# Optimization experiments

Hardware: AMD Instinct MI355X
Metric: run time of the kernel (lower is better)

Reference implementation:

```python
import jax, jax.numpy as jnp
import numpy as np

B, C, INTER, H, W = 8, 256, 128, 64, 64

def setup_inputs() -> dict:
    key = jax.random.key(0)
    ks = jax.random.split(key, 9)
    s = 0.02
    return {
        "x": jax.random.normal(ks[0], (B, C, H, W), dtype=jnp.float32),
        "Wg": jax.random.normal(ks[1], (INTER, C), dtype=jnp.float32) * s,
        "bg": jax.random.normal(ks[2], (INTER,), dtype=jnp.float32) * s,
        "Wt": jax.random.normal(ks[3], (INTER, C), dtype=jnp.float32) * s,
        "bt": jax.random.normal(ks[4], (INTER,), dtype=jnp.float32) * s,
        "Wp": jax.random.normal(ks[5], (INTER, C), dtype=jnp.float32) * s,
        "bp": jax.random.normal(ks[6], (INTER,), dtype=jnp.float32) * s,
        "Wm": jax.random.normal(ks[7], (C, INTER), dtype=jnp.float32) * s,
        "bm": jax.random.normal(ks[8], (C,), dtype=jnp.float32) * s,
    }

def reference(x, Wg, bg, Wt, bt, Wp, bp, Wm, bm):
    # x: [B, C, H, W]; 1x1 convs are channel GEMMs.
    b, c, h, w = x.shape
    n = h * w
    def conv1x1(inp, Wc, bc):
        return jnp.einsum('bchw,oc->bohw', inp, Wc) + bc[None, :, None, None]
    g_x = conv1x1(x, Wg, bg).reshape(b, -1, n).transpose(0, 2, 1)      # [B, N, d]
    theta_x = conv1x1(x, Wt, bt).reshape(b, -1, n).transpose(0, 2, 1)  # [B, N, d]
    phi_x = conv1x1(x, Wp, bp).reshape(b, -1, n)                       # [B, d, N]
    scores = jnp.einsum('bnd,bdm->bnm', theta_x, phi_x)               # [B, N, N]
    attn = jax.nn.softmax(scores, axis=-1)
    y = jnp.einsum('bnm,bmd->bnd', attn, g_x)                          # [B, N, d]
    y = y.transpose(0, 2, 1).reshape(b, -1, h, w)                      # [B, d, H, W]
    mask = conv1x1(y, Wm, bm)                                          # [B, C, H, W]
    return mask + x
```

## Files before the change

### kernel.cpp

```cpp
#include <hip/hip_runtime.h>
#include <hip/hip_bf16.h>
#include <math.h>

#define BATCH 8
#define CH    256
#define DIM   128
#define NSP   4096

using bf16 = __hip_bfloat16;
typedef __attribute__((ext_vector_type(8))) short bf16x8;
typedef __attribute__((ext_vector_type(4))) float f32x4;

__device__ __forceinline__ unsigned short f2b(float f) {
  return __builtin_bit_cast(unsigned short, __float2bfloat16(f));
}

__device__ __forceinline__ float fexp2(float x) {
  float r;
  asm("v_exp_f32 %0, %1" : "=v"(r) : "v"(x));
  return r;
}

__device__ __forceinline__ void gload16(const void* g, void* l) {
  __builtin_amdgcn_global_load_lds(
      (const __attribute__((address_space(1))) unsigned int*)g,
      (__attribute__((address_space(3))) unsigned int*)l, 16, 0, 0);
}

__global__ __launch_bounds__(256) void k_weights(const float* __restrict__ Wg,
                                                 const float* __restrict__ Wt,
                                                 const float* __restrict__ Wp,
                                                 const float* __restrict__ Wm,
                                                 bf16* __restrict__ Wcat,
                                                 bf16* __restrict__ Wmb) {
  int i = blockIdx.x * 256 + threadIdx.x;
  if (i < 3 * DIM * CH) {
    const float* src = (i < 32768) ? Wg : (i < 65536 ? Wt : Wp);
    Wcat[i] = __float2bfloat16(src[i & 32767]);
  }
  if (i < CH * DIM) Wmb[i] = __float2bfloat16(Wm[i]);
}

__global__ __launch_bounds__(256) void k_transpose(const float* __restrict__ x,
                                                   bf16* __restrict__ xbT) {
  __shared__ __align__(16) float tile[64][68];
  const int b = blockIdx.z, ct = blockIdx.y, nt = blockIdx.x;
  const int t = threadIdx.x;
  const int tr = t >> 4;
  const int tc = t & 15;
  const float* src = x + ((size_t)b * CH + ct * 64) * NSP + nt * 64;
  #pragma unroll
  for (int p = 0; p < 4; ++p) {
    int c = p * 16 + tr;
    float4 v = *(const float4*)(src + (size_t)c * NSP + tc * 4);
    *(float4*)(&tile[c][tc * 4]) = v;
  }
  __syncthreads();
  bf16* dst = xbT + ((size_t)b * NSP + nt * 64) * CH + ct * 64;
  #pragma unroll
  for (int p = 0; p < 4; ++p) {
    int n = p * 16 + tr;
    ushort4 pk;
    pk.x = f2b(tile[tc * 4 + 0][n]);
    pk.y = f2b(tile[tc * 4 + 1][n]);
    pk.z = f2b(tile[tc * 4 + 2][n]);
    pk.w = f2b(tile[tc * 4 + 3][n]);
    *(ushort4*)(dst + (size_t)n * CH + tc * 4) = pk;
  }
}

__global__ __launch_bounds__(256) void k_proj(const bf16* __restrict__ Wcat,
                                              const bf16* __restrict__ xbT,
                                              const float* __restrict__ bg,
                                              const float* __restrict__ bt,
                                              const float* __restrict__ bp,
                                              bf16* __restrict__ theta,
                                              bf16* __restrict__ phi,
                                              bf16* __restrict__ gT) {
  __shared__ __align__(16) char lds[32768];
  const int b = blockIdx.z, p = blockIdx.y, nt = blockIdx.x;
  const int tid = threadIdx.x;
  const int l = tid & 63, w = tid >> 6;
  const int wm = w >> 1, wn = w & 1;
  const int lr = l & 15, lh = l >> 4;
  const int ldsw = (tid & ~63) << 4;

  f32x4 acc[4][4];
  #pragma unroll
  for (int i = 0; i < 4; ++i)
    #pragma unroll
    for (int j = 0; j < 4; ++j) acc[i][j] = (f32x4){0.f, 0.f, 0.f, 0.f};

  const bf16* Asrc = Wcat + (size_t)p * DIM * CH;
  const bf16* Bsrc = xbT + ((size_t)b * NSP + nt * 128) * CH;

  for (int kt = 0; kt < 4; ++kt) {
    const int k0 = kt * 64;
    #pragma unroll
    for (int cc = 0; cc < 4; ++cc) {
      int t = cc * 256 + tid;
      int row = t >> 3, g = t & 7;
      gload16(Asrc + (size_t)row * CH + k0 + ((g ^ (row & 7)) << 3),
              lds + cc * 4096 + ldsw);
      gload16(Bsrc + (size_t)row * CH + k0 + ((g ^ (row & 7)) << 3),
              lds + 16384 + cc * 4096 + ldsw);
    }
    __syncthreads();
    #pragma unroll
    for (int kk = 0; kk < 2; ++kk) {
      bf16x8 af[4], bfr[4];
      #pragma unroll
      for (int mf = 0; mf < 4; ++mf) {
        int row = wm * 64 + mf * 16 + lr;
        int g = kk * 4 + lh;
        af[mf] = *(const bf16x8*)(lds + row * 128 + ((g ^ (row & 7)) << 4));
      }
      #pragma unroll
      for (int nf = 0; nf < 4; ++nf) {
        int row = wn * 64 + nf * 16 + lr;
        int g = kk * 4 + lh;
        bfr[nf] = *(const bf16x8*)(lds + 16384 + row * 128 + ((g ^ (row & 7)) << 4));
      }
      #pragma unroll
      for (int mf = 0; mf < 4; ++mf)
        #pragma unroll
        for (int nf = 0; nf < 4; ++nf)
          acc[mf][nf] = __builtin_amdgcn_mfma_f32_16x16x32_bf16(af[mf], bfr[nf],
                                                                acc[mf][nf], 0, 0, 0);
    }
    __syncthreads();
  }

  const float* bias = (p == 0) ? bg : (p == 1 ? bt : bp);
  bf16* nd = (p == 1) ? theta : phi;
  const float oscale = (p == 1) ? 1.44269504088896f : 1.0f;
  #pragma unroll
  for (int mf = 0; mf < 4; ++mf) {
    const int dbase = wm * 64 + mf * 16 + lh * 4;
    const float4 bv = *(const float4*)(bias + dbase);
    float bvv[4] = {bv.x, bv.y, bv.z, bv.w};
    #pragma unroll
    for (int nf = 0; nf < 4; ++nf) {
      const int n = nt * 128 + wn * 64 + nf * 16 + lr;
      float v[4];
      #pragma unroll
      for (int r = 0; r < 4; ++r) v[r] = (acc[mf][nf][r] + bvv[r]) * oscale;
      if (p == 0) {
        #pragma unroll
        for (int r = 0; r < 4; ++r)
          gT[((size_t)b * DIM + dbase + r) * NSP + n] = __float2bfloat16(v[r]);
      } else {
        ushort4 pk;
        pk.x = f2b(v[0]); pk.y = f2b(v[1]); pk.z = f2b(v[2]); pk.w = f2b(v[3]);
        *(ushort4*)(nd + ((size_t)b * NSP + n) * DIM + dbase) = pk;
      }
    }
  }
}

__global__ __launch_bounds__(512, 2) void k_attn(const bf16* __restrict__ theta,
                                                 const bf16* __restrict__ phi,
                                                 const bf16* __restrict__ gT,
                                                 bf16* __restrict__ y) {
  __shared__ __align__(16) char lds[131072];
  const int b = blockIdx.y, qt = blockIdx.x;
  const int tid = threadIdx.x;
  const int l = tid & 63, w = tid >> 6;
  const int h = w >> 2;
  const int p = w & 3;
  const int lr = l & 15, lh = l >> 4;
  const int tid_h = tid & 255;
  const int ldsw_h = (tid_h & ~63) << 4;

  bf16x8 qf[2][4];
  #pragma unroll
  for (int g = 0; g < 2; ++g) {
    const bf16* qsrc =
        theta + ((size_t)(b * NSP + qt * 128 + p * 32 + g * 16 + lr)) * DIM + lh * 8;
    #pragma unroll
    for (int f = 0; f < 4; ++f) qf[g][f] = *(const bf16x8*)(qsrc + f * 32);
  }

  f32x4 o[2][8];
  #pragma unroll
  for (int g = 0; g < 2; ++g)
    #pragma unroll
    for (int dt = 0; dt < 8; ++dt) o[g][dt] = (f32x4){0.f, 0.f, 0.f, 0.f};
  f32x4 den[2];
  den[0] = (f32x4){0.f, 0.f, 0.f, 0.f};
  den[1] = (f32x4){0.f, 0.f, 0.f, 0.f};

  bf16x8 vones;
  #pragma unroll
  for (int j = 0; j < 8; ++j) vones[j] = (short)0x3F80;

  const bf16* Ksrc = phi + (size_t)b * NSP * DIM;
  const bf16* Vsrc = gT + (size_t)b * DIM * NSP;
  const int kvbase = h * 2048;
  char* const ldsh = lds + h * 65536;

  const bf16* kp[4];
  const bf16* vp[4];
  #pragma unroll
  for (int cc = 0; cc < 4; ++cc) {
    int t = cc * 256 + tid_h;
    int row = t >> 4, g = t & 15;
    int kvs = (row & 32) | (((row >> 2) & 3) << 3) | (((row >> 4) & 1) << 2) |
              (row & 3);
    kp[cc] = Ksrc + (size_t)(kvbase + kvs) * DIM + ((g ^ (row & 7)) << 3);
    int row2 = t >> 3, g2 = t & 7;
    vp[cc] = Vsrc + (size_t)row2 * NSP + kvbase + ((g2 ^ (row2 & 7)) << 3);
  }

  auto stage = [&](int buf) {
    #pragma unroll
    for (int cc = 0; cc < 4; ++cc) {
      gload16(kp[cc], ldsh + buf * 16384 + cc * 4096 + ldsw_h);
      gload16(vp[cc], ldsh + 32768 + buf * 16384 + cc * 4096 + ldsw_h);
      kp[cc] += 64 * DIM;
      vp[cc] += 64;
    }
  };

  stage(0);

  for (int it = 0; it < 32; ++it) {
    if (it < 31) {
      stage((it + 1) & 1);
      asm volatile("s_waitcnt vmcnt(8)" ::: "memory");
    } else {
      asm volatile("s_waitcnt vmcnt(0)" ::: "memory");
    }
    __builtin_amdgcn_s_barrier();
    __builtin_amdgcn_sched_barrier(0);

    const char* Kb = ldsh + (it & 1) * 16384;
    const char* Vb = ldsh + 32768 + (it & 1) * 16384;

    f32x4 sa[2][4];
    #pragma unroll
    for (int g = 0; g < 2; ++g)
      #pragma unroll
      for (int ct = 0; ct < 4; ++ct) sa[g][ct] = (f32x4){0.f, 0.f, 0.f, 0.f};
    #pragma unroll
    for (int ct = 0; ct < 4; ++ct) {
      const int row = ct * 16 + lr;
      #pragma unroll
      for (int f = 0; f < 4; ++f) {
        const int g = f * 4 + lh;
        bf16x8 kf = *(const bf16x8*)(Kb + row * 256 + ((g ^ (row & 7)) << 4));
        sa[0][ct] = __builtin_amdgcn_mfma_f32_16x16x32_bf16(kf, qf[0][f], sa[0][ct], 0, 0, 0);
        sa[1][ct] = __builtin_amdgcn_mfma_f32_16x16x32_bf16(kf, qf[1][f], sa[1][ct], 0, 0, 0);
      }
    }

    #pragma unroll
    for (int ct = 0; ct < 4; ++ct)
      #pragma unroll
      for (int r = 0; r < 4; ++r) {
        sa[0][ct][r] = fexp2(sa[0][ct][r]);
        sa[1][ct][r] = fexp2(sa[1][ct][r]);
      }

    bf16x8 pf[2][2];
    #pragma unroll
    for (int g = 0; g < 2; ++g)
      #pragma unroll
      for (int c = 0; c < 2; ++c) {
        union { bf16x8 v; unsigned short u[8]; } pw;
        #pragma unroll
        for (int u = 0; u < 2; ++u)
          #pragma unroll
          for (int r = 0; r < 4; ++r) pw.u[u * 4 + r] = f2b(sa[g][2 * c + u][r]);
        pf[g][c] = pw.v;
      }

    #pragma unroll
    for (int c = 0; c < 2; ++c) {
      const int gp = c * 4 + lh;
      den[0] = __builtin_amdgcn_mfma_f32_16x16x32_bf16(pf[0][c], vones, den[0], 0, 0, 0);
      den[1] = __builtin_amdgcn_mfma_f32_16x16x32_bf16(pf[1][c], vones, den[1], 0, 0, 0);
      #pragma unroll
      for (int dt = 0; dt < 8; ++dt) {
        const int row = dt * 16 + lr;
        bf16x8 vf = *(const bf16x8*)(Vb + row * 128 + ((gp ^ (row & 7)) << 4));
        o[0][dt] = __builtin_amdgcn_mfma_f32_16x16x32_bf16(pf[0][c], vf, o[0][dt], 0, 0, 0);
        o[1][dt] = __builtin_amdgcn_mfma_f32_16x16x32_bf16(pf[1][c], vf, o[1][dt], 0, 0, 0);
      }
    }

    asm volatile("s_waitcnt lgkmcnt(0)" ::: "memory");
    __builtin_amdgcn_s_barrier();
  }

  {
    #pragma unroll
    for (int g = 0; g < 2; ++g) {
      char* slot = lds + (size_t)((p * 2 + g) * 64 + l) * 144;
      if (h == 1) {
        #pragma unroll
        for (int dt = 0; dt < 8; ++dt) *(f32x4*)(slot + dt * 16) = o[g][dt];
        *(f32x4*)(slot + 128) = den[g];
      }
    }
    __syncthreads();
    if (h == 0) {
      #pragma unroll
      for (int g = 0; g < 2; ++g) {
        char* slot = lds + (size_t)((p * 2 + g) * 64 + l) * 144;
        const f32x4 db = *(const f32x4*)(slot + 128);
        float inv[4];
        #pragma unroll
        for (int r = 0; r < 4; ++r) inv[r] = 1.f / (den[g][r] + db[r]);
        #pragma unroll
        for (int dt = 0; dt < 8; ++dt) {
          const f32x4 ob = *(const f32x4*)(slot + dt * 16);
          const int d = dt * 16 + lr;
          #pragma unroll
          for (int r = 0; r < 4; ++r) {
            const int q = qt * 128 + p * 32 + g * 16 + lh * 4 + r;
            y[(size_t)(b * NSP + q) * DIM + d] =
                __float2bfloat16((o[g][dt][r] + ob[r]) * inv[r]);
          }
        }
      }
    }
  }
}

__global__ __launch_bounds__(256) void k_final(const bf16* __restrict__ Wmb,
                                               const bf16* __restrict__ yb,
                                               const float* __restrict__ bm,
                                               const float* __restrict__ x,
                                               float* __restrict__ out) {
  __shared__ __align__(16) char lds[32768];
  const int b = blockIdx.z, mt = blockIdx.y, nt = blockIdx.x;
  const int tid = threadIdx.x;
  const int l = tid & 63, w = tid >> 6;
  const int wm = w >> 1, wn = w & 1;
  const int lr = l & 15, lh = l >> 4;
  const int ldsw = (tid & ~63) << 4;

  f32x4 acc[4][4];
  #pragma unroll
  for (int i = 0; i < 4; ++i)
    #pragma unroll
    for (int j = 0; j < 4; ++j) acc[i][j] = (f32x4){0.f, 0.f, 0.f, 0.f};

  const bf16* Asrc = Wmb + (size_t)mt * 128 * DIM;
  const bf16* Bsrc = yb + ((size_t)b * NSP + nt * 128) * DIM;

  for (int kt = 0; kt < 2; ++kt) {
    const int k0 = kt * 64;
    #pragma unroll
    for (int cc = 0; cc < 4; ++cc) {
      int t = cc * 256 + tid;
      int row = t >> 3, g = t & 7;
      gload16(Asrc + (size_t)row * DIM + k0 + ((g ^ (row & 7)) << 3),
              lds + cc * 4096 + ldsw);
      gload16(Bsrc + (size_t)row * DIM + k0 + ((g ^ (row & 7)) << 3),
              lds + 16384 + cc * 4096 + ldsw);
    }
    __syncthreads();
    #pragma unroll
    for (int kk = 0; kk < 2; ++kk) {
      bf16x8 af[4], bfr[4];
      #pragma unroll
      for (int mf = 0; mf < 4; ++mf) {
        int row = wm * 64 + mf * 16 + lr;
        int g = kk * 4 + lh;
        af[mf] = *(const bf16x8*)(lds + row * 128 + ((g ^ (row & 7)) << 4));
      }
      #pragma unroll
      for (int nf = 0; nf < 4; ++nf) {
        int row = wn * 64 + nf * 16 + lr;
        int g = kk * 4 + lh;
        bfr[nf] = *(const bf16x8*)(lds + 16384 + row * 128 + ((g ^ (row & 7)) << 4));
      }
      #pragma unroll
      for (int mf = 0; mf < 4; ++mf)
        #pragma unroll
        for (int nf = 0; nf < 4; ++nf)
          acc[mf][nf] = __builtin_amdgcn_mfma_f32_16x16x32_bf16(af[mf], bfr[nf],
                                                                acc[mf][nf], 0, 0, 0);
    }
    __syncthreads();
  }

  #pragma unroll
  for (int mf = 0; mf < 4; ++mf) {
    const int cbase = mt * 128 + wm * 64 + mf * 16 + lh * 4;
    const float4 bv = *(const float4*)(bm + cbase);
    float bvv[4] = {bv.x, bv.y, bv.z, bv.w};
    #pragma unroll
    for (int nf = 0; nf < 4; ++nf) {
      const int n = nt * 128 + wn * 64 + nf * 16 + lr;
      #pragma unroll
      for (int r = 0; r < 4; ++r) {
        const size_t idx = ((size_t)b * CH + cbase + r) * NSP + n;
        out[idx] = acc[mf][nf][r] + bvv[r] + x[idx];
      }
    }
  }
}

extern "C" void kernel_launch(void* const* d_in, const int* in_sizes, int n_in,
                              void* d_out, int out_size, void* d_ws, size_t ws_size,
                              hipStream_t stream) {
  const float* x  = (const float*)d_in[0];
  const float* Wg = (const float*)d_in[1];
  const float* bg = (const float*)d_in[2];
  const float* Wt = (const float*)d_in[3];
  const float* bt = (const float*)d_in[4];
  const float* Wp = (const float*)d_in[5];
  const float* bp = (const float*)d_in[6];
  const float* Wm = (const float*)d_in[7];
  const float* bm = (const float*)d_in[8];
  float* out = (float*)d_out;
  char* ws = (char*)d_ws;

  bf16* xbT   = (bf16*)(ws + 0);
  bf16* Wcat  = (bf16*)(ws + 16777216);
  bf16* Wmb   = (bf16*)(ws + 16973824);
  bf16* theta = (bf16*)(ws + 17039360);
  bf16* phi   = (bf16*)(ws + 25427968);
  bf16* gT    = (bf16*)(ws + 33816576);
  bf16* yb    = (bf16*)(ws + 42205184);

  k_weights  <<<dim3(384),       dim3(256), 0, stream>>>(Wg, Wt, Wp, Wm, Wcat, Wmb);
  k_transpose<<<dim3(64, 4, 8),  dim3(256), 0, stream>>>(x, xbT);
  k_proj     <<<dim3(32, 3, 8),  dim3(256), 0, stream>>>(Wcat, xbT, bg, bt, bp,
                                                         theta, phi, gT);
  k_attn     <<<dim3(32, 8),     dim3(512), 0, stream>>>(theta, phi, gT, yb);
  k_final    <<<dim3(32, 2, 8),  dim3(256), 0, stream>>>(Wmb, yb, bm, x, out);
}
```

Baseline: 199.9 us.

## Fuse weight cast into transpose, reuse x tile across projections, single-stage final GEMM

The weight-conversion kernel is folded into the transpose kernel as an extra z-slice of blocks, which saves one launch. The projection kernel now loads each x tile into LDS once and loops over the three projections, reusing it instead of launching three separate blocks per tile. This cuts the grid from 768 to 256 blocks and raises LDS to 80KB, which may hurt occupancy and parallelism. The final GEMM loads the whole K=128 extent in one stage, dropping one sync round but doubling LDS use.

```diff
diff --git a/kernel.cpp b/kernel.cpp
--- a/kernel.cpp
+++ b/kernel.cpp
@@ -27,22 +27,31 @@
       (__attribute__((address_space(3))) unsigned int*)l, 16, 0, 0);
 }
 
-__global__ __launch_bounds__(256) void k_weights(const float* __restrict__ Wg,
-                                                 const float* __restrict__ Wt,
-                                                 const float* __restrict__ Wp,
-                                                 const float* __restrict__ Wm,
-                                                 bf16* __restrict__ Wcat,
-                                                 bf16* __restrict__ Wmb) {
-  int i = blockIdx.x * 256 + threadIdx.x;
-  if (i < 3 * DIM * CH) {
-    const float* src = (i < 32768) ? Wg : (i < 65536 ? Wt : Wp);
-    Wcat[i] = __float2bfloat16(src[i & 32767]);
-  }
-  if (i < CH * DIM) Wmb[i] = __float2bfloat16(Wm[i]);
-}
-
 __global__ __launch_bounds__(256) void k_transpose(const float* __restrict__ x,
-                                                   bf16* __restrict__ xbT) {
+                                                   bf16* __restrict__ xbT,
+                                                   const float* __restrict__ Wg,
+                                                   const float* __restrict__ Wt,
+                                                   const float* __restrict__ Wp,
+                                                   const float* __restrict__ Wm,
+                                                   bf16* __restrict__ Wcat,
+                                                   bf16* __restrict__ Wmb) {
+  if (blockIdx.z == 8) {
+    int id = (blockIdx.y * 64 + blockIdx.x) * 256 + threadIdx.x;
+    int i2 = id * 2;
+    if (i2 < 3 * DIM * CH) {
+      #pragma unroll
+      for (int e = 0; e < 2; ++e) {
+        int i = i2 + e;
+        const float* src = (i < 32768) ? Wg : (i < 65536 ? Wt : Wp);
+        Wcat[i] = __float2bfloat16(src[i & 32767]);
+      }
+    } else {
+      int k = i2 - 3 * DIM * CH;
+      Wmb[k]     = __float2bfloat16(Wm[k]);
+      Wmb[k + 1] = __float2bfloat16(Wm[k + 1]);
+    }
+    return;
+  }
   __shared__ __align__(16) float tile[64][68];
   const int b = blockIdx.z, ct = blockIdx.y, nt = blockIdx.x;
   const int t = threadIdx.x;
@@ -77,82 +86,91 @@
                                               bf16* __restrict__ theta,
                                               bf16* __restrict__ phi,
                                               bf16* __restrict__ gT) {
-  __shared__ __align__(16) char lds[32768];
-  const int b = blockIdx.z, p = blockIdx.y, nt = blockIdx.x;
+  __shared__ __align__(16) char lds[81920];
+  const int b = blockIdx.y, nt = blockIdx.x;
   const int tid = threadIdx.x;
   const int l = tid & 63, w = tid >> 6;
   const int wm = w >> 1, wn = w & 1;
   const int lr = l & 15, lh = l >> 4;
   const int ldsw = (tid & ~63) << 4;
 
-  f32x4 acc[4][4];
-  #pragma unroll
-  for (int i = 0; i < 4; ++i)
-    #pragma unroll
-    for (int j = 0; j < 4; ++j) acc[i][j] = (f32x4){0.f, 0.f, 0.f, 0.f};
-
-  const bf16* Asrc = Wcat + (size_t)p * DIM * CH;
   const bf16* Bsrc = xbT + ((size_t)b * NSP + nt * 128) * CH;
 
-  for (int kt = 0; kt < 4; ++kt) {
-    const int k0 = kt * 64;
+  #pragma unroll
+  for (int kt = 0; kt < 4; ++kt)
     #pragma unroll
     for (int cc = 0; cc < 4; ++cc) {
       int t = cc * 256 + tid;
       int row = t >> 3, g = t & 7;
-      gload16(Asrc + (size_t)row * CH + k0 + ((g ^ (row & 7)) << 3),
-              lds + cc * 4096 + ldsw);
-      gload16(Bsrc + (size_t)row * CH + k0 + ((g ^ (row & 7)) << 3),
-              lds + 16384 + cc * 4096 + ldsw);
-    }
-    __syncthreads();
-    #pragma unroll
-    for (int kk = 0; kk < 2; ++kk) {
-      bf16x8 af[4], bfr[4];
-      #pragma unroll
-      for (int mf = 0; mf < 4; ++mf) {
-        int row = wm * 64 + mf * 16 + lr;
-        int g = kk * 4 + lh;
-        af[mf] = *(const bf16x8*)(lds + row * 128 + ((g ^ (row & 7)) << 4));
-      }
+      gload16(Bsrc + (size_t)row * CH + kt * 64 + ((g ^ (row & 7)) << 3),
+              lds + kt * 16384 + cc * 4096 + ldsw);
+    }
+
+  for (int p = 0; p < 3; ++p) {
+    f32x4 acc[4][4];
+    #pragma unroll
+    for (int i = 0; i < 4; ++i)
+      #pragma unroll
+      for (int j = 0; j < 4; ++j) acc[i][j] = (f32x4){0.f, 0.f, 0.f, 0.f};
+    const bf16* Asrc = Wcat + (size_t)p * DIM * CH;
+
+    for (int kt = 0; kt < 4; ++kt) {
+      __syncthreads();
+      #pragma unroll
+      for (int cc = 0; cc < 4; ++cc) {
+        int t = cc * 256 + tid;
+        int row = t >> 3, g = t & 7;
+        gload16(Asrc + (size_t)row * CH + kt * 64 + ((g ^ (row & 7)) << 3),
+                lds + 65536 + cc * 4096 + ldsw);
+      }
+      __syncthreads();
+      #pragma unroll
+      for (int kk = 0; kk < 2; ++kk) {
+        bf16x8 af[4], bfr[4];
+        #pragma unroll
+        for (int mf = 0; mf < 4; ++mf) {
+          int row = wm * 64 + mf * 16 + lr;
+          int g = kk * 4 + lh;
+          af[mf] = *(const bf16x8*)(lds + 65536 + row * 128 + ((g ^ (row & 7)) << 4));
+        }
+        #pragma unroll
+        for (int nf = 0; nf < 4; ++nf) {
+          int row = wn * 64 + nf * 16 + lr;
+          int g = kk * 4 + lh;
+          bfr[nf] = *(const bf16x8*)(lds + kt * 16384 + row * 128 + ((g ^ (row & 7)) << 4));
+        }
+        #pragma unroll
+        for (int mf = 0; mf < 4; ++mf)
+          #pragma unroll
+          for (int nf = 0; nf < 4; ++nf)
+            acc[mf][nf] = __builtin_amdgcn_mfma_f32_16x16x32_bf16(af[mf], bfr[nf],
+                                                                  acc[mf][nf], 0, 0, 0);
+      }
+    }
+
+    const float* bias = (p == 0) ? bg : (p == 1 ? bt : bp);
+    bf16* nd = (p == 1) ? theta : phi;
+    const float oscale = (p == 1) ? 1.44269504088896f : 1.0f;
+    #pragma unroll
+    for (int mf = 0; mf < 4; ++mf) {
+      const int dbase = wm * 64 + mf * 16 + lh * 4;
+      const float4 bv = *(const float4*)(bias + dbase);
+      float bvv[4] = {bv.x, bv.y, bv.z, bv.w};
       #pragma unroll
       for (int nf = 0; nf < 4; ++nf) {
-        int row = wn * 64 + nf * 16 + lr;
-        int g = kk * 4 + lh;
-        bfr[nf] = *(const bf16x8*)(lds + 16384 + row * 128 + ((g ^ (row & 7)) << 4));
-      }
-      #pragma unroll
-      for (int mf = 0; mf < 4; ++mf)
-        #pragma unroll
-        for (int nf = 0; nf < 4; ++nf)
-          acc[mf][nf] = __builtin_amdgcn_mfma_f32_16x16x32_bf16(af[mf], bfr[nf],
-                                                                acc[mf][nf], 0, 0, 0);
-    }
-    __syncthreads();
-  }
-
-  const float* bias = (p == 0) ? bg : (p == 1 ? bt : bp);
-  bf16* nd = (p == 1) ? theta : phi;
-  const float oscale = (p == 1) ? 1.44269504088896f : 1.0f;
-  #pragma unroll
-  for (int mf = 0; mf < 4; ++mf) {
-    const int dbase = wm * 64 + mf * 16 + lh * 4;
-    const float4 bv = *(const float4*)(bias + dbase);
-    float bvv[4] = {bv.x, bv.y, bv.z, bv.w};
-    #pragma unroll
-    for (int nf = 0; nf < 4; ++nf) {
-      const int n = nt * 128 + wn * 64 + nf * 16 + lr;
-      float v[4];
-      #pragma unroll
-      for (int r = 0; r < 4; ++r) v[r] = (acc[mf][nf][r] + bvv[r]) * oscale;
-      if (p == 0) {
-        #pragma unroll
-        for (int r = 0; r < 4; ++r)
-          gT[((size_t)b * DIM + dbase + r) * NSP + n] = __float2bfloat16(v[r]);
-      } else {
-        ushort4 pk;
-        pk.x = f2b(v[0]); pk.y = f2b(v[1]); pk.z = f2b(v[2]); pk.w = f2b(v[3]);
-        *(ushort4*)(nd + ((size_t)b * NSP + n) * DIM + dbase) = pk;
+        const int n = nt * 128 + wn * 64 + nf * 16 + lr;
+        float v[4];
+        #pragma unroll
+        for (int r = 0; r < 4; ++r) v[r] = (acc[mf][nf][r] + bvv[r]) * oscale;
+        if (p == 0) {
+          #pragma unroll
+          for (int r = 0; r < 4; ++r)
+            gT[((size_t)b * DIM + dbase + r) * NSP + n] = __float2bfloat16(v[r]);
+        } else {
+          ushort4 pk;
+          pk.x = f2b(v[0]); pk.y = f2b(v[1]); pk.z = f2b(v[2]); pk.w = f2b(v[3]);
+          *(ushort4*)(nd + ((size_t)b * NSP + n) * DIM + dbase) = pk;
+        }
       }
     }
   }
@@ -333,7 +351,7 @@
                                                const float* __restrict__ bm,
                                                const float* __restrict__ x,
                                                float* __restrict__ out) {
-  __shared__ __align__(16) char lds[32768];
+  __shared__ __align__(16) char lds[65536];
   const int b = blockIdx.z, mt = blockIdx.y, nt = blockIdx.x;
   const int tid = threadIdx.x;
   const int l = tid & 63, w = tid >> 6;
@@ -341,50 +359,47 @@
   const int lr = l & 15, lh = l >> 4;
   const int ldsw = (tid & ~63) << 4;
 
-  f32x4 acc[4][4];
-  #pragma unroll
-  for (int i = 0; i < 4; ++i)
-    #pragma unroll
-    for (int j = 0; j < 4; ++j) acc[i][j] = (f32x4){0.f, 0.f, 0.f, 0.f};
-
   const bf16* Asrc = Wmb + (size_t)mt * 128 * DIM;
   const bf16* Bsrc = yb + ((size_t)b * NSP + nt * 128) * DIM;
 
-  for (int kt = 0; kt < 2; ++kt) {
-    const int k0 = kt * 64;
-    #pragma unroll
-    for (int cc = 0; cc < 4; ++cc) {
-      int t = cc * 256 + tid;
-      int row = t >> 3, g = t & 7;
-      gload16(Asrc + (size_t)row * DIM + k0 + ((g ^ (row & 7)) << 3),
-              lds + cc * 4096 + ldsw);
-      gload16(Bsrc + (size_t)row * DIM + k0 + ((g ^ (row & 7)) << 3),
-              lds + 16384 + cc * 4096 + ldsw);
-    }
-    __syncthreads();
-    #pragma unroll
-    for (int kk = 0; kk < 2; ++kk) {
-      bf16x8 af[4], bfr[4];
-      #pragma unroll
-      for (int mf = 0; mf < 4; ++mf) {
-        int row = wm * 64 + mf * 16 + lr;
-        int g = kk * 4 + lh;
-        af[mf] = *(const bf16x8*)(lds + row * 128 + ((g ^ (row & 7)) << 4));
-      }
-      #pragma unroll
-      for (int nf = 0; nf < 4; ++nf) {
-        int row = wn * 64 + nf * 16 + lr;
-        int g = kk * 4 + lh;
-        bfr[nf] = *(const bf16x8*)(lds + 16384 + row * 128 + ((g ^ (row & 7)) << 4));
-      }
-      #pragma unroll
-      for (int mf = 0; mf < 4; ++mf)
-        #pragma unroll
-        for (int nf = 0; nf < 4; ++nf)
-          acc[mf][nf] = __builtin_amdgcn_mfma_f32_16x16x32_bf16(af[mf], bfr[nf],
-                                                                acc[mf][nf], 0, 0, 0);
-    }
-    __syncthreads();
+  #pragma unroll
+  for (int cc = 0; cc < 8; ++cc) {
+    int t = cc * 256 + tid;
+    int row = t >> 4, g = t & 15;
+    gload16(Asrc + (size_t)row * DIM + ((g ^ (row & 7)) << 3),
+            lds + cc * 4096 + ldsw);
+    gload16(Bsrc + (size_t)row * DIM + ((g ^ (row & 7)) << 3),
+            lds + 32768 + cc * 4096 + ldsw);
+  }
+  __syncthreads();
+
+  f32x4 acc[4][4];
+  #pragma unroll
+  for (int i = 0; i < 4; ++i)
+    #pragma unroll
+    for (int j = 0; j < 4; ++j) acc[i][j] = (f32x4){0.f, 0.f, 0.f, 0.f};
+
+  #pragma unroll
+  for (int kk = 0; kk < 4; ++kk) {
+    bf16x8 af[4], bfr[4];
+    #pragma unroll
+    for (int mf = 0; mf < 4; ++mf) {
+      int row = wm * 64 + mf * 16 + lr;
+      int g = kk * 4 + lh;
+      af[mf] = *(const bf16x8*)(lds + row * 256 + ((g ^ (row & 7)) << 4));
+    }
+    #pragma unroll
+    for (int nf = 0; nf < 4; ++nf) {
+      int row = wn * 64 + nf * 16 + lr;
+      int g = kk * 4 + lh;
+      bfr[nf] = *(const bf16x8*)(lds + 32768 + row * 256 + ((g ^ (row & 7)) << 4));
+    }
+    #pragma unroll
+    for (int mf = 0; mf < 4; ++mf)
+      #pragma unroll
+      for (int nf = 0; nf < 4; ++nf)
+        acc[mf][nf] = __builtin_amdgcn_mfma_f32_16x16x32_bf16(af[mf], bfr[nf],
+                                                              acc[mf][nf], 0, 0, 0);
   }
 
   #pragma unroll
@@ -427,9 +442,9 @@
   bf16* gT    = (bf16*)(ws + 33816576);
   bf16* yb    = (bf16*)(ws + 42205184);
 
-  k_weights  <<<dim3(384),       dim3(256), 0, stream>>>(Wg, Wt, Wp, Wm, Wcat, Wmb);
-  k_transpose<<<dim3(64, 4, 8),  dim3(256), 0, stream>>>(x, xbT);
-  k_proj     <<<dim3(32, 3, 8),  dim3(256), 0, stream>>>(Wcat, xbT, bg, bt, bp,
+  k_transpose<<<dim3(64, 4, 9),  dim3(256), 0, stream>>>(x, xbT, Wg, Wt, Wp, Wm,
+                                                         Wcat, Wmb);
+  k_proj     <<<dim3(32, 8),     dim3(256), 0, stream>>>(Wcat, xbT, bg, bt, bp,
                                                          theta, phi, gT);
   k_attn     <<<dim3(32, 8),     dim3(512), 0, stream>>>(theta, phi, gT, yb);
   k_final    <<<dim3(32, 2, 8),  dim3(256), 0, stream>>>(Wmb, yb, bm, x, out);
```

Measured after the change: 194.9 us. 1.03x faster.
